# Kernel optimization log

Measured on AMD Instinct MI355X. Metric: run time of the kernel, lower is better.

## Reference

```python
import jax, jax.numpy as jnp
import numpy as np

N = 38332          # poi_len - 1 nodes
POI_LEN = 38333
GF = 64            # graph_features
POI_DIM = 128
C = 128            # gcn_channel
L = 4              # gcn_layers
OUT = 128          # graph_out_dim
E = N * 16         # edges (avg degree 16)
IN_DIM = POI_DIM * GF // 2 + GF // 2  # 4128


def leaky(x, s):
    return jnp.where(x >= 0, x, s * x)


def _gcn(x, W, b, src, dst):
    # PyG GCNConv: lin -> symmetric deg^{-1/2} norm over self-loop graph -> scatter-sum + bias
    h = x @ W
    deg = jax.ops.segment_sum(jnp.ones(src.shape[0], h.dtype), dst, num_segments=N)
    dinv = jnp.where(deg > 0, jax.lax.rsqrt(deg), 0.0)
    norm = dinv[src] * dinv[dst]
    return jax.ops.segment_sum(h[src] * norm[:, None], dst, num_segments=N) + b


def _gat(x, W, a_src, a_dst, b, src, dst):
    # PyG GATConv (heads=1): per-edge LeakyReLU(0.2) logits, softmax over incoming edges
    h = x @ W
    als = h @ a_src            # [N]
    ald = h @ a_dst            # [N]
    e = leaky(als[src] + ald[dst], 0.2)   # [E+N]
    m = jax.ops.segment_max(e, dst, num_segments=N)
    ex = jnp.exp(e - m[dst])
    s = jax.ops.segment_sum(ex, dst, num_segments=N)
    alpha = ex / s[dst]
    return jax.ops.segment_sum(h[src] * alpha[:, None], dst, num_segments=N) + b


def _gnorm(x, w, b, ms, eps=1e-5):
    # PyG GraphNorm over the single graph (node axis)
    mean = x.mean(axis=0)
    out = x - ms * mean
    var = (out * out).mean(axis=0)
    return w * out * jax.lax.rsqrt(var + eps) + b


def setup_inputs() -> dict:
    key = jax.random.key(0)
    ks = jax.random.split(key, 20)
    d = {}
    d["poi"] = jax.random.randint(ks[0], (N, GF // 2), 0, POI_LEN, dtype=jnp.int32)
    d["distance"] = jax.random.uniform(ks[1], (N, GF // 2), dtype=jnp.float32)
    d["edge_index"] = jax.random.randint(ks[2], (2, E), 0, N, dtype=jnp.int32)
    d["emb_table"] = jax.random.normal(ks[3], (POI_LEN, POI_DIM), dtype=jnp.float32) * 0.05
    d["W_in"] = jax.random.normal(ks[4], (IN_DIM, C), dtype=jnp.float32) * 0.02
    d["b_in"] = jnp.zeros((C,), jnp.float32)
    d["gcn_W"] = jax.random.normal(ks[5], (L, C, C), dtype=jnp.float32) * 0.05
    d["gcn_b"] = jnp.zeros((L, C), jnp.float32)
    d["norm_w"] = jnp.ones((L, C), jnp.float32)
    d["norm_b"] = jnp.zeros((L, C), jnp.float32)
    d["norm_ms"] = jnp.ones((L, C), jnp.float32)
    d["gat_W"] = jax.random.normal(ks[6], (L, C, C), dtype=jnp.float32) * 0.05
    d["gat_asrc"] = jax.random.normal(ks[7], (L, C), dtype=jnp.float32) * 0.05
    d["gat_adst"] = jax.random.normal(ks[8], (L, C), dtype=jnp.float32) * 0.05
    d["gat_b"] = jnp.zeros((L, C), jnp.float32)
    d["W_out"] = jax.random.normal(ks[9], (C, 1), dtype=jnp.float32) * 0.05
    d["b_out"] = jnp.zeros((1,), jnp.float32)
    d["fc1_W"] = jax.random.normal(ks[10], (N, 128), dtype=jnp.float32) * 0.01
    d["fc1_b"] = jnp.zeros((128,), jnp.float32)
    d["fc2_W"] = jax.random.normal(ks[11], (128, OUT), dtype=jnp.float32) * 0.05
    d["fc2_b"] = jnp.zeros((OUT,), jnp.float32)
    return d


def reference(poi, distance, edge_index, emb_table, W_in, b_in, gcn_W, gcn_b,
              norm_w, norm_b, norm_ms, gat_W, gat_asrc, gat_adst, gat_b,
              W_out, b_out, fc1_W, fc1_b, fc2_W, fc2_b):
    loops = jnp.arange(N, dtype=edge_index.dtype)
    src = jnp.concatenate([edge_index[0], loops])   # self loops (PyG default)
    dst = jnp.concatenate([edge_index[1], loops])
    # feature assembly: emb(poi) flattened || distance
    x = jnp.concatenate([emb_table[poi].reshape(N, -1), distance], axis=1)  # [N, 4128]
    x = leaky(_gcn(x, W_in, b_in, src, dst), 0.01)
    for i in range(L):  # GcnUnit: GCN->norm->lrelu->res, GAT->norm->lrelu->res (shared norm params)
        t = _gnorm(_gcn(x, gcn_W[i], gcn_b[i], src, dst), norm_w[i], norm_b[i], norm_ms[i])
        x = x + leaky(t, 0.01)
        t = _gnorm(_gat(x, gat_W[i], gat_asrc[i], gat_adst[i], gat_b[i], src, dst),
                   norm_w[i], norm_b[i], norm_ms[i])
        x = x + leaky(t, 0.01)
    x = leaky(_gcn(x, W_out, b_out, src, dst), 0.01).reshape(-1)  # [N]
    h = leaky(x @ fc1_W + fc1_b, 0.01)
    return h @ fc2_W + fc2_b  # [128]
```

## Files before the change

### kernel.cpp

```cpp
#include <hip/hip_runtime.h>


typedef _Float16 f16;
typedef f16 f16x8 __attribute__((ext_vector_type(8)));
typedef f16 f16x4 __attribute__((ext_vector_type(4)));
typedef f16 f16x2 __attribute__((ext_vector_type(2)));
typedef float f32x4 __attribute__((ext_vector_type(4)));

__device__ __forceinline__ float lrelu(float x, float s){ return x>=0.f? x : s*x; }

__global__ __launch_bounds__(256) void k_deg(const int* __restrict__ dst,
                                             int* __restrict__ deg, int E) {
  int i = blockIdx.x * 256 + threadIdx.x;
  if (i < E) atomicAdd(&deg[dst[i]], 1);
}

__global__ __launch_bounds__(1024) void k_scan1(const int* __restrict__ deg,
    int* __restrict__ row_ptr, int* __restrict__ bsum, float* __restrict__ dinv, int n) {
  int b = blockIdx.x, t = threadIdx.x, i = b * 1024 + t;
  __shared__ int sd[1024];
  int v = (i < n) ? deg[i] : 0;
  if (i < n) dinv[i] = rsqrtf((float)(v + 1));
  sd[t] = v;
  __syncthreads();
  for (int off = 1; off < 1024; off <<= 1) {
    int o = (t >= off) ? sd[t - off] : 0;
    __syncthreads();
    sd[t] += o;
    __syncthreads();
  }
  if (i < n) row_ptr[i + 1] = sd[t];
  if (t == 1023) bsum[b] = sd[1023];
  if (b == 0 && t == 0) row_ptr[0] = 0;
}

__global__ __launch_bounds__(64) void k_scan2(int* __restrict__ bsum, int nb) {
  int lane = threadIdx.x;
  int v = (lane < nb) ? bsum[lane] : 0;
  int x = v;
  for (int off = 1; off < 64; off <<= 1) {
    int o = __shfl_up(x, off, 64);
    if (lane >= off) x += o;
  }
  if (lane < nb) bsum[lane] = x - v;
}

__global__ __launch_bounds__(256) void k_scan3(int* __restrict__ row_ptr,
                                               const int* __restrict__ bsum, int n) {
  int i = blockIdx.x * 256 + threadIdx.x;
  if (i < n) row_ptr[i + 1] += bsum[i >> 10];
}

__global__ __launch_bounds__(256) void k_fill(const int* __restrict__ src,
                                              const int* __restrict__ dst,
                                              const int* __restrict__ row_ptr,
                                              const float* __restrict__ dinv,
                                              int* __restrict__ fill,
                                              int* __restrict__ csr,
                                              float* __restrict__ csrw, int E) {
  int i = blockIdx.x * 256 + threadIdx.x;
  if (i < E) {
    int d = dst[i], s = src[i];
    int pos = row_ptr[d] + atomicAdd(&fill[d], 1);
    csr[pos] = s;
    csrw[pos] = dinv[d] * dinv[s];
  }
}

__global__ __launch_bounds__(256) void k_conv_emb(const float* __restrict__ src,
                                                  f16* __restrict__ dst, int total4) {
  int i = blockIdx.x * 256 + threadIdx.x;
  if (i >= total4) return;
  float4 v = ((const float4*)src)[i];
  f16x4 o = { (f16)v.x, (f16)v.y, (f16)v.z, (f16)v.w };
  ((f16x4*)dst)[i] = o;
}

__global__ __launch_bounds__(256) void k_pack_w(const float* __restrict__ W,
    f16* __restrict__ hi, int kb_total) {
  int idx = blockIdx.x * 256 + threadIdx.x;
  int c = idx & 127, kb = idx >> 7;
  if (kb >= kb_total) return;
  f16x8 hv;
#pragma unroll
  for (int j = 0; j < 8; j++) hv[j] = (f16)W[(size_t)(kb*8 + j) * 128 + c];
  ((f16x8*)hi)[idx] = hv;
}

__global__ __launch_bounds__(256) void k_pack_w8(const float* __restrict__ gcnW,
    const float* __restrict__ gatW, f16* __restrict__ hi, f16* __restrict__ lo) {
  int mat = blockIdx.y;
  const float* W = (mat < 4) ? gcnW + (size_t)mat * 16384 : gatW + (size_t)(mat - 4) * 16384;
  int idx = blockIdx.x * 256 + threadIdx.x;
  int c = idx & 127, kb = idx >> 7;
  f16x8 hv, lv;
#pragma unroll
  for (int j = 0; j < 8; j++) {
    float v = W[(size_t)(kb*8 + j) * 128 + c];
    f16 h = (f16)v;
    hv[j] = h; lv[j] = (f16)(v - (float)h);
  }
  ((f16x8*)hi)[mat * 2048 + idx] = hv;
  ((f16x8*)lo)[mat * 2048 + idx] = lv;
}

#define APAD 152
__global__ __launch_bounds__(512) void k_mfma_embed(const int* __restrict__ poi,
    const float* __restrict__ dist, const f16* __restrict__ eh,
    const f16* __restrict__ wh, f16* __restrict__ H16, int n) {
  __shared__ __attribute__((aligned(16))) char smem[49152];
  int* poi_s = (int*)smem;
  f16* aS    = (f16*)(smem + 8192);
  f16* OT    = (f16*)smem;
  float* F   = (float*)(smem + 16384);
  int tid = threadIdx.x;
  int bn = blockIdx.x * 64;
  int half = tid >> 8;
  int t2 = tid & 255;
  int ln = t2 >> 2, qt = t2 & 3;
  int xrow = bn + ln; if (xrow > n - 1) xrow = n - 1;
  {
#pragma unroll
    for (int jj = 0; jj < 4; jj++)
      poi_s[half * 1024 + (qt * 4 + jj) * 64 + ln] =
        poi[(size_t)xrow * 32 + half * 16 + qt * 4 + jj];
  }
  int w2 = (tid >> 6) & 3, lane = tid & 63;
  int q = lane >> 4, l15 = lane & 15;
  int mtb = (w2 & 1) * 2;
  int ntb = (w2 >> 1) * 4;
  f16* aH = aS + half * 64 * APAD;
  f32x4 acc[2][4];
#pragma unroll
  for (int a = 0; a < 2; a++)
#pragma unroll
    for (int b = 0; b < 4; b++) { acc[a][b][0]=0.f; acc[a][b][1]=0.f; acc[a][b][2]=0.f; acc[a][b][3]=0.f; }
  __syncthreads();

  f16x8 r0, r1, r2, r3;
  {
    const f16* srcp = eh + (size_t)poi_s[half * 1024 + ln] * 128 + qt * 32;
    r0 = *(const f16x8*)(srcp);      r1 = *(const f16x8*)(srcp + 8);
    r2 = *(const f16x8*)(srcp + 16); r3 = *(const f16x8*)(srcp + 24);
  }

#pragma unroll 1
  for (int j = 0; j < 16; j++) {
    __syncthreads();
    f16* wp = aH + ln * APAD + qt * 32;
    *(f16x8*)(wp) = r0; *(f16x8*)(wp + 8) = r1;
    *(f16x8*)(wp + 16) = r2; *(f16x8*)(wp + 24) = r3;
    if (j + 1 < 16) {
      const f16* srcp = eh + (size_t)poi_s[half * 1024 + (j + 1) * 64 + ln] * 128 + qt * 32;
      r0 = *(const f16x8*)(srcp);      r1 = *(const f16x8*)(srcp + 8);
      r2 = *(const f16x8*)(srcp + 16); r3 = *(const f16x8*)(srcp + 24);
    }
    __syncthreads();
#pragma unroll
    for (int kcl = 0; kcl < 4; kcl++) {
      f16x8 a_h[2];
#pragma unroll
      for (int mi = 0; mi < 2; mi++)
        a_h[mi] = *(const f16x8*)(aH + ((mtb + mi) * 16 + l15) * APAD + kcl * 32 + q * 8);
      int kb = (half * 16 + j) * 16 + kcl * 4 + q;
#pragma unroll
      for (int ni = 0; ni < 4; ni++) {
        f16x8 bh = *(const f16x8*)(wh + ((size_t)kb * 128 + (ntb + ni) * 16 + l15) * 8);
#pragma unroll
        for (int mi = 0; mi < 2; mi++)
          acc[mi][ni] = __builtin_amdgcn_mfma_f32_16x16x32_f16(a_h[mi], bh, acc[mi][ni], 0, 0, 0);
      }
    }
  }
  if (half) {
    int nc0 = bn + (mtb + 0) * 16 + l15; if (nc0 > n - 1) nc0 = n - 1;
    int nc1 = bn + (mtb + 1) * 16 + l15; if (nc1 > n - 1) nc1 = n - 1;
    f16x8 ad[2];
#pragma unroll
    for (int mi = 0; mi < 2; mi++) {
      int nc = mi ? nc1 : nc0;
      const float* dp = dist + (size_t)nc * 32 + q * 8;
      float4 d0 = *(const float4*)dp, d1 = *(const float4*)(dp + 4);
      ad[mi][0]=(f16)d0.x; ad[mi][1]=(f16)d0.y; ad[mi][2]=(f16)d0.z; ad[mi][3]=(f16)d0.w;
      ad[mi][4]=(f16)d1.x; ad[mi][5]=(f16)d1.y; ad[mi][6]=(f16)d1.z; ad[mi][7]=(f16)d1.w;
    }
    int kb = 512 + q;
#pragma unroll
    for (int ni = 0; ni < 4; ni++) {
      f16x8 bh = *(const f16x8*)(wh + ((size_t)kb * 128 + (ntb + ni) * 16 + l15) * 8);
#pragma unroll
      for (int mi = 0; mi < 2; mi++)
        acc[mi][ni] = __builtin_amdgcn_mfma_f32_16x16x32_f16(ad[mi], bh, acc[mi][ni], 0, 0, 0);
    }
  }
  __syncthreads();
  if (half) {
#pragma unroll
    for (int mi = 0; mi < 2; mi++)
#pragma unroll
      for (int ni = 0; ni < 4; ni++)
#pragma unroll
        for (int r = 0; r < 4; r++)
          F[((mtb + mi) * 16 + q * 4 + r) * 128 + (ntb + ni) * 16 + l15] = acc[mi][ni][r];
  }
  __syncthreads();
  if (!half) {
#pragma unroll
    for (int mi = 0; mi < 2; mi++)
#pragma unroll
      for (int ni = 0; ni < 4; ni++)
#pragma unroll
        for (int r = 0; r < 4; r++) {
          int o = ((mtb + mi) * 16 + q * 4 + r) * 128 + (ntb + ni) * 16 + l15;
          OT[o] = (f16)(acc[mi][ni][r] + F[o]);
        }
  }
  __syncthreads();
#pragma unroll
  for (int ch = 0; ch < 2; ch++) {
    int c1024 = tid + ch * 512;
    int row = c1024 >> 4, c8 = c1024 & 15;
    if (bn + row < n)
      *(f16x8*)(H16 + (size_t)(bn + row) * 128 + c8 * 8) = *(const f16x8*)(OT + row * 128 + c8 * 8);
  }
}

#define LPAD 136
__global__ __launch_bounds__(256) void k_mfma_lin(const f16* __restrict__ XH,
    const f16* __restrict__ wh, const f16* __restrict__ wl,
    f16* __restrict__ H16, int n,
    const float* __restrict__ asrc, const float* __restrict__ adst,
    float* __restrict__ als, float* __restrict__ ald,
    const float* __restrict__ yres, const float* __restrict__ ps,
    const float* __restrict__ pq, const float* __restrict__ nw,
    const float* __restrict__ nbb, const float* __restrict__ nms,
    float* __restrict__ xf) {
  __shared__ __attribute__((aligned(16))) char smem[64 * LPAD * 2 + 3072];
  f16* aS = (f16*)smem;
  f16* ot = (f16*)smem;
  float* dsrc = (float*)(smem + 16384);
  float* ddst = (float*)(smem + 16896);
  float* scf  = (float*)(smem + 17408);
  float* shf  = scf + 128;
  float* sst1 = (float*)(smem + 18432);
  float* sst2 = sst1 + 256;
  int tid = threadIdx.x;
  int bn = blockIdx.x * 64;
  int ln = tid >> 2, qt = tid & 3;
  int w = tid >> 6, lane = tid & 63;
  int q = lane >> 4, l15 = lane & 15;
  int mtb = (w & 1) * 2;
  int ntb = (w >> 1) * 4;
  f16* wp = aS + ln * LPAD + qt * 32;
  if (yres) {
    {
      int c = tid & 127, hf = tid >> 7;
      float S = 0.f, Q = 0.f;
      for (int s = hf; s < 128; s += 2) { S += ps[s * 128 + c]; Q += pq[s * 128 + c]; }
      sst1[tid] = S; sst2[tid] = Q;
      __syncthreads();
      if (hf == 0) {
        double Sd = (double)sst1[c] + (double)sst1[c + 128];
        double Qd = (double)sst2[c] + (double)sst2[c + 128];
        double invn = 1.0 / (double)n;
        double mean = Sd * invn;
        double mt = (double)nms[c] * mean;
        double var = Qd * invn - 2.0 * mt * mean + mt * mt;
        float rstd = rsqrtf((float)var + 1e-5f);
        float sc = nw[c] * rstd;
        scf[c] = sc;
        shf[c] = nbb[c] - sc * (float)mt;
      }
      __syncthreads();
    }
    int row = bn + ln;
    if (row < n) {
      const float4* yp = (const float4*)(yres + (size_t)row * 128 + qt * 32);
      float4* xp = (float4*)(xf + (size_t)row * 128 + qt * 32);
      const float4* scp = (const float4*)(scf + qt * 32);
      const float4* shp = (const float4*)(shf + qt * 32);
#pragma unroll
      for (int jj = 0; jj < 8; jj++) {
        float4 yv = yp[jj], xv = xp[jj], sc = scp[jj], sh = shp[jj];
        xv.x += lrelu(sc.x * yv.x + sh.x, 0.01f);
        xv.y += lrelu(sc.y * yv.y + sh.y, 0.01f);
        xv.z += lrelu(sc.z * yv.z + sh.z, 0.01f);
        xv.w += lrelu(sc.w * yv.w + sh.w, 0.01f);
        xp[jj] = xv;
        f16x4 o = { (f16)xv.x, (f16)xv.y, (f16)xv.z, (f16)xv.w };
        *(f16x4*)(wp + jj * 4) = o;
      }
    } else {
      f16x8 z = {};
#pragma unroll
      for (int jj = 0; jj < 4; jj++) *(f16x8*)(wp + jj * 8) = z;
    }
  } else {
    int xrow = bn + ln; if (xrow > n - 1) xrow = n - 1;
    const f16* srcp = XH + (size_t)xrow * 128 + qt * 32;
    *(f16x8*)(wp)      = *(const f16x8*)(srcp);
    *(f16x8*)(wp + 8)  = *(const f16x8*)(srcp + 8);
    *(f16x8*)(wp + 16) = *(const f16x8*)(srcp + 16);
    *(f16x8*)(wp + 24) = *(const f16x8*)(srcp + 24);
  }
  float av[4], bv[4];
  if (asrc) {
#pragma unroll
    for (int ni = 0; ni < 4; ni++) {
      av[ni] = asrc[(ntb + ni) * 16 + l15];
      bv[ni] = adst[(ntb + ni) * 16 + l15];
    }
  }
  f32x4 acc[2][4];
#pragma unroll
  for (int a = 0; a < 2; a++)
#pragma unroll
    for (int b = 0; b < 4; b++) { acc[a][b][0]=0.f; acc[a][b][1]=0.f; acc[a][b][2]=0.f; acc[a][b][3]=0.f; }
  __syncthreads();
#pragma unroll
  for (int kcl = 0; kcl < 4; kcl++) {
    f16x8 a_h[2];
#pragma unroll
    for (int mi = 0; mi < 2; mi++)
      a_h[mi] = *(const f16x8*)(aS + ((mtb + mi) * 16 + l15) * LPAD + kcl * 32 + q * 8);
    int kb = kcl * 4 + q;
#pragma unroll
    for (int ni = 0; ni < 4; ni++) {
      size_t boff = ((size_t)kb * 128 + (ntb + ni) * 16 + l15) * 8;
      f16x8 bh = *(const f16x8*)(wh + boff);
      f16x8 bl = *(const f16x8*)(wl + boff);
#pragma unroll
      for (int mi = 0; mi < 2; mi++) {
        acc[mi][ni] = __builtin_amdgcn_mfma_f32_16x16x32_f16(a_h[mi], bh, acc[mi][ni], 0, 0, 0);
        acc[mi][ni] = __builtin_amdgcn_mfma_f32_16x16x32_f16(a_h[mi], bl, acc[mi][ni], 0, 0, 0);
      }
    }
  }
  __syncthreads();
  if (asrc) {
#pragma unroll
    for (int mi = 0; mi < 2; mi++)
#pragma unroll
      for (int r = 0; r < 4; r++) {
        float ps2 = 0.f, pd = 0.f;
#pragma unroll
        for (int ni = 0; ni < 4; ni++) { ps2 += acc[mi][ni][r] * av[ni]; pd += acc[mi][ni][r] * bv[ni]; }
#pragma unroll
        for (int msk = 8; msk > 0; msk >>= 1) {
          ps2 += __shfl_xor(ps2, msk, 64);
          pd += __shfl_xor(pd, msk, 64);
        }
        if (l15 == 0) {
          int row = (mtb + mi) * 16 + q * 4 + r;
          dsrc[row * 2 + (w >> 1)] = ps2;
          ddst[row * 2 + (w >> 1)] = pd;
        }
      }
  }
#pragma unroll
  for (int mi = 0; mi < 2; mi++)
#pragma unroll
    for (int ni = 0; ni < 4; ni++)
#pragma unroll
      for (int r = 0; r < 4; r++)
        ot[((mtb + mi) * 16 + q * 4 + r) * 128 + (ntb + ni) * 16 + l15] = (f16)acc[mi][ni][r];
  __syncthreads();
  if (bn + ln < n) {
    f16* dst = H16 + (size_t)(bn + ln) * 128 + qt * 32;
    const f16* srcp = ot + ln * 128 + qt * 32;
#pragma unroll
    for (int jj = 0; jj < 4; jj++)
      *(f16x8*)(dst + jj * 8) = *(const f16x8*)(srcp + jj * 8);
  }
  if (asrc && tid < 64 && bn + tid < n) {
    als[bn + tid] = dsrc[tid * 2] + dsrc[tid * 2 + 1];
    ald[bn + tid] = ddst[tid * 2] + ddst[tid * 2 + 1];
  }
}

__global__ __launch_bounds__(256) void k_gcn_agg16(const f16x2* __restrict__ H2,
    const float* __restrict__ dinv, const int* __restrict__ row_ptr,
    const int* __restrict__ csr, const float* __restrict__ csrw,
    const float* __restrict__ bias,
    float2* __restrict__ out2, f16x2* __restrict__ xh_out, int n, int leaky_flag,
    float* __restrict__ psum, float* __restrict__ psumsq) {
  int w = threadIdx.x >> 6;
  int node = blockIdx.x * 4 + w;
  int lane = threadIdx.x & 63;
  __shared__ float s1[4][128], s2[4][128];
  float vx = 0.f, vy = 0.f;
  if (node < n) {
    int rs = row_ptr[node], re = row_ptr[node + 1];
    int d = re - rs;
    float dn = dinv[node];
    int  sidx = (lane < d) ? csr[rs + lane]  : 0;
    float swt = (lane < d) ? csrw[rs + lane] : 0.f;
    f16x2 sv = H2[(size_t)node * 64 + lane];
    float ax = dn * dn * (float)sv[0], ay = dn * dn * (float)sv[1];
    int dl = d < 64 ? d : 64;
    int dl8 = (dl + 7) & ~7;
    for (int j = 0; j < dl8; j += 8) {
      int ii[8]; float ww[8];
#pragma unroll
      for (int u = 0; u < 8; u++) {
        ii[u] = __shfl(sidx, j + u, 64);
        ww[u] = __shfl(swt,  j + u, 64);
      }
      f16x2 vv[8];
#pragma unroll
      for (int u = 0; u < 8; u++) vv[u] = H2[(size_t)ii[u] * 64 + lane];
#pragma unroll
      for (int u = 0; u < 8; u++) {
        ax += ww[u] * (float)vv[u][0];
        ay += ww[u] * (float)vv[u][1];
      }
    }
    for (int e = rs + 64; e < re; e++) {
      int s = csr[e]; float wv = csrw[e];
      f16x2 v = H2[(size_t)s * 64 + lane];
      ax += wv * (float)v[0]; ay += wv * (float)v[1];
    }
    float2 bvv = ((const float2*)bias)[lane];
    vx = ax + bvv.x; vy = ay + bvv.y;
    if (leaky_flag) { vx = lrelu(vx, 0.01f); vy = lrelu(vy, 0.01f); }
    out2[(size_t)node * 64 + lane] = make_float2(vx, vy);
    if (xh_out) { f16x2 o = { (f16)vx, (f16)vy }; xh_out[(size_t)node * 64 + lane] = o; }
  }
  if (psum) {
    s1[w][2*lane] = vx;  s1[w][2*lane+1] = vy;
    s2[w][2*lane] = vx*vx; s2[w][2*lane+1] = vy*vy;
    __syncthreads();
    int t = threadIdx.x;
    if (t < 128) {
      float S = s1[0][t] + s1[1][t] + s1[2][t] + s1[3][t];
      float Q = s2[0][t] + s2[1][t] + s2[2][t] + s2[3][t];
      int slot = blockIdx.x & 127;
      atomicAdd(&psum[slot * 128 + t], S);
      atomicAdd(&psumsq[slot * 128 + t], Q);
    }
  }
}

__global__ __launch_bounds__(256) void k_gat_agg16(const f16x2* __restrict__ H2,
    const float* __restrict__ als, const float* __restrict__ ald,
    const int* __restrict__ row_ptr, const int* __restrict__ csr,
    const float* __restrict__ bias, float2* __restrict__ y2, int n,
    float* __restrict__ psum, float* __restrict__ psumsq) {
  int w = threadIdx.x >> 6;
  int node = blockIdx.x * 4 + w;
  int lane = threadIdx.x & 63;
  __shared__ float s1[4][128], s2[4][128];
  float vx = 0.f, vy = 0.f;
  if (node < n) {
    int rs = row_ptr[node], re = row_ptr[node + 1];
    int d = re - rs;
    float aldn = ald[node];
    float e_self = lrelu(als[node] + aldn, 0.2f);
    f16x2 sv = H2[(size_t)node * 64 + lane];
    float ax, ay, sm;
    if (d <= 64) {
      int sidx = (lane < d) ? csr[rs + lane] : 0;
      float e_k = (lane < d) ? lrelu(als[sidx] + aldn, 0.2f) : -3.4e38f;
      float tmx = e_k;
      for (int off = 1; off < 64; off <<= 1) tmx = fmaxf(tmx, __shfl_xor(tmx, off, 64));
      float mx = fmaxf(e_self, tmx);
      float g_k = (lane < d) ? __expf(e_k - mx) : 0.f;
      float tsm = g_k;
      for (int off = 1; off < 64; off <<= 1) tsm += __shfl_xor(tsm, off, 64);
      float ws = __expf(e_self - mx);
      sm = tsm + ws;
      ax = ws * (float)sv[0]; ay = ws * (float)sv[1];
      int d8 = (d + 7) & ~7;
      for (int j = 0; j < d8; j += 8) {
        int ii[8]; float gg[8];
#pragma unroll
        for (int u = 0; u < 8; u++) {
          ii[u] = __shfl(sidx, j + u, 64);
          gg[u] = __shfl(g_k,  j + u, 64);
        }
        f16x2 vv[8];
#pragma unroll
        for (int u = 0; u < 8; u++) vv[u] = H2[(size_t)ii[u] * 64 + lane];
#pragma unroll
        for (int u = 0; u < 8; u++) {
          ax += gg[u] * (float)vv[u][0];
          ay += gg[u] * (float)vv[u][1];
        }
      }
    } else {
      float mx = e_self;
      for (int i = rs + lane; i < re; i += 64) mx = fmaxf(mx, lrelu(als[csr[i]] + aldn, 0.2f));
      for (int off = 1; off < 64; off <<= 1) mx = fmaxf(mx, __shfl_xor(mx, off, 64));
      float ws = __expf(e_self - mx);
      sm = ws;
      ax = ws * (float)sv[0]; ay = ws * (float)sv[1];
      for (int i = rs; i < re; i++) {
        int s = csr[i];
        float g = __expf(lrelu(als[s] + aldn, 0.2f) - mx);
        f16x2 v = H2[(size_t)s * 64 + lane];
        sm += g; ax += g*(float)v[0]; ay += g*(float)v[1];
      }
    }
    float inv_s = 1.f / sm;
    float2 bvv = ((const float2*)bias)[lane];
    vx = ax * inv_s + bvv.x; vy = ay * inv_s + bvv.y;
    y2[(size_t)node * 64 + lane] = make_float2(vx, vy);
  }
  s1[w][2*lane] = vx;  s1[w][2*lane+1] = vy;
  s2[w][2*lane] = vx*vx; s2[w][2*lane+1] = vy*vy;
  __syncthreads();
  int t = threadIdx.x;
  if (t < 128) {
    float S = s1[0][t] + s1[1][t] + s1[2][t] + s1[3][t];
    float Q = s2[0][t] + s2[1][t] + s2[2][t] + s2[3][t];
    int slot = blockIdx.x & 127;
    atomicAdd(&psum[slot * 128 + t], S);
    atomicAdd(&psumsq[slot * 128 + t], Q);
  }
}

__global__ __launch_bounds__(256) void k_stats(const float* __restrict__ psum,
    const float* __restrict__ psumsq, const float* __restrict__ w,
    const float* __restrict__ bb, const float* __restrict__ ms,
    float* __restrict__ scaleA, float* __restrict__ shiftA, int n) {
  int t = threadIdx.x, c = t & 127, half = t >> 7;
  float S = 0.f, Q = 0.f;
  for (int s = half; s < 128; s += 2) { S += psum[s * 128 + c]; Q += psumsq[s * 128 + c]; }
  __shared__ float sh[256], sq[256];
  sh[t] = S; sq[t] = Q;
  __syncthreads();
  if (half == 0) {
    double Sd = (double)sh[c] + (double)sh[c + 128];
    double Qd = (double)sq[c] + (double)sq[c + 128];
    double invn = 1.0 / (double)n;
    double mean = Sd * invn;
    double mt = (double)ms[c] * mean;
    double var = Qd * invn - 2.0 * mt * mean + mt * mt;
    float rstd = rsqrtf((float)var + 1e-5f);
    float sc = w[c] * rstd;
    scaleA[c] = sc;
    shiftA[c] = bb[c] - sc * (float)mt;
  }
}

__global__ __launch_bounds__(256) void k_dot1_res(const float* __restrict__ y,
    const float* __restrict__ scA, const float* __restrict__ shA,
    const float* __restrict__ x, const float* __restrict__ wv,
    float* __restrict__ o, int n) {
  int node = blockIdx.x * 4 + (threadIdx.x >> 6);
  int lane = threadIdx.x & 63;
  if (node >= n) return;
  float2 yv = ((const float2*)y)[(size_t)node * 64 + lane];
  float2 xv = ((const float2*)x)[(size_t)node * 64 + lane];
  float2 sc = ((const float2*)scA)[lane];
  float2 sh = ((const float2*)shA)[lane];
  float hx = xv.x + lrelu(sc.x * yv.x + sh.x, 0.01f);
  float hy = xv.y + lrelu(sc.y * yv.y + sh.y, 0.01f);
  float2 v1 = ((const float2*)wv)[lane];
  float s1 = hx * v1.x + hy * v1.y;
  for (int off = 32; off > 0; off >>= 1) s1 += __shfl_down(s1, off, 64);
  if (lane == 0) o[node] = s1;
}

__global__ __launch_bounds__(256) void k_scalar_agg(const float* __restrict__ xsv,
    const float* __restrict__ dinv, const int* __restrict__ row_ptr,
    const int* __restrict__ csr, const float* __restrict__ csrw,
    const float* __restrict__ b_out, float* __restrict__ xout, int n) {
  int i = blockIdx.x * 256 + threadIdx.x;
  if (i >= n) return;
  float dn = dinv[i];
  float acc = dn * dn * xsv[i];
  int re = row_ptr[i + 1];
  for (int e = row_ptr[i]; e < re; e++)
    acc += csrw[e] * xsv[csr[e]];
  xout[i] = lrelu(acc + b_out[0], 0.01f);
}

__global__ __launch_bounds__(256) void k_fc1(const float* __restrict__ xout,
    const float* __restrict__ fw, float* __restrict__ pfc, int n, int chunk) {
  int b = blockIdx.x, t = threadIdx.x;
  int c = t & 127, half = t >> 7;
  int s0 = b * chunk;
  int s1 = s0 + chunk; if (s1 > n) s1 = n;
  float s = 0.f;
  for (int i = s0 + half; i < s1; i += 2) s += xout[i] * fw[(size_t)i * 128 + c];
  __shared__ float sh[256];
  sh[t] = s; __syncthreads();
  if (half == 0) pfc[b * 128 + c] = sh[c] + sh[c + 128];
}

__global__ __launch_bounds__(128) void k_final(const float* __restrict__ pfc,
    const float* __restrict__ b1, const float* __restrict__ fw2,
    const float* __restrict__ b2, float* __restrict__ out) {
  int c = threadIdx.x;
  float s = 0.f;
  for (int b = 0; b < 128; b++) s += pfc[b * 128 + c];
  float hv = lrelu(s + b1[c], 0.01f);
  __shared__ float h1[128];
  h1[c] = hv; __syncthreads();
  float o = b2[c];
  for (int j = 0; j < 128; j++) o += h1[j] * fw2[j * 128 + c];
  out[c] = o;
}

extern "C" void kernel_launch(void* const* d_in, const int* in_sizes, int n_in,
                              void* d_out, int out_size, void* d_ws, size_t ws_size,
                              hipStream_t stream) {
  const int* poi      = (const int*)d_in[0];
  const float* dist   = (const float*)d_in[1];
  const int* ei       = (const int*)d_in[2];
  const float* emb    = (const float*)d_in[3];
  const float* W_in   = (const float*)d_in[4];
  const float* b_in   = (const float*)d_in[5];
  const float* gcn_W  = (const float*)d_in[6];
  const float* gcn_b  = (const float*)d_in[7];
  const float* norm_w = (const float*)d_in[8];
  const float* norm_b = (const float*)d_in[9];
  const float* norm_ms= (const float*)d_in[10];
  const float* gat_W  = (const float*)d_in[11];
  const float* gat_as = (const float*)d_in[12];
  const float* gat_ad = (const float*)d_in[13];
  const float* gat_b  = (const float*)d_in[14];
  const float* W_out  = (const float*)d_in[15];
  const float* b_out  = (const float*)d_in[16];
  const float* fc1_W  = (const float*)d_in[17];
  const float* fc1_b  = (const float*)d_in[18];
  const float* fc2_W  = (const float*)d_in[19];
  const float* fc2_b  = (const float*)d_in[20];

  const int N   = in_sizes[0] / 32;
  const int E   = in_sizes[2] / 2;
  const int POI = in_sizes[3] / 128;
  const int* srcp = ei;
  const int* dstp = ei + E;
  float* out = (float*)d_out;

  char* p = (char*)d_ws;
  auto alloc = [&](size_t bytes) { char* r = p; p += (bytes + 255) & ~(size_t)255; return r; };
  float* x   = (float*)alloc((size_t)N * 128 * 4);
  f16* h16   = (f16*)alloc((size_t)N * 128 * 2);
  f16* xh    = (f16*)alloc((size_t)N * 128 * 2);
  size_t Rneed = (size_t)POI * 128 * 2;
  size_t Ry    = (size_t)N * 128 * 4;
  char* R = alloc(Rneed > Ry ? Rneed : Ry);
  f16* ehalf = (f16*)R;
  float* y   = (float*)R;
  const int KBIN = 4128 / 8;
  f16* wih = (f16*)alloc((size_t)KBIN * 128 * 8 * 2);
  f16* wsh = (f16*)alloc((size_t)8 * 16384 * 2);
  f16* wsl = (f16*)alloc((size_t)8 * 16384 * 2);
  float* dinv   = (float*)alloc((size_t)N * 4);
  float* als    = (float*)alloc((size_t)N * 4);
  float* ald    = (float*)alloc((size_t)N * 4);
  float* xsv    = (float*)alloc((size_t)N * 4);
  float* xout   = (float*)alloc((size_t)N * 4);
  float* statsbuf = (float*)alloc((size_t)32 * 16384 * 4);
  float* pfc    = (float*)alloc(128 * 128 * 4);
  float* scaleA = (float*)alloc(128 * 4);
  float* shiftA = (float*)alloc(128 * 4);
  int* deg     = (int*)alloc((size_t)N * 2 * 4);
  int* fill    = deg + N;
  int* row_ptr = (int*)alloc(((size_t)N + 1) * 4);
  int* csr     = (int*)alloc((size_t)E * 4);
  float* csrw  = (float*)alloc((size_t)E * 4);
  int* bsum    = (int*)alloc(64 * 4);

  const int chunk = (N + 127) / 128;
  const int gblocks = (N + 63) / 64;
  const int eblocks = (E + 255) / 256;
  const int nwb = (N + 3) / 4;
  const int nb1024 = (N + 1023) / 1024;

  hipMemsetAsync(deg, 0, sizeof(int) * 2 * (size_t)N, stream);
  hipMemsetAsync(statsbuf, 0, (size_t)32 * 16384 * 4, stream);
  k_deg<<<eblocks, 256, 0, stream>>>(dstp, deg, E);
  k_scan1<<<nb1024, 1024, 0, stream>>>(deg, row_ptr, bsum, dinv, N);
  k_scan2<<<1, 64, 0, stream>>>(bsum, nb1024);
  k_scan3<<<(N + 255) / 256, 256, 0, stream>>>(row_ptr, bsum, N);
  k_fill<<<eblocks, 256, 0, stream>>>(srcp, dstp, row_ptr, dinv, fill, csr, csrw, E);

  int et4 = POI * 128 / 4;
  k_conv_emb<<<(et4 + 255) / 256, 256, 0, stream>>>(emb, ehalf, et4);
  k_pack_w<<<(KBIN * 128 + 255) / 256, 256, 0, stream>>>(W_in, wih, KBIN);
  k_pack_w8<<<dim3(8, 8), 256, 0, stream>>>(gcn_W, gat_W, wsh, wsl);

  k_mfma_embed<<<gblocks, 512, 0, stream>>>(poi, dist, ehalf, wih, h16, N);
  k_gcn_agg16<<<nwb, 256, 0, stream>>>((const f16x2*)h16, dinv, row_ptr, csr, csrw, b_in,
                                       (float2*)x, (f16x2*)xh, N, 1, nullptr, nullptr);

  for (int l = 0; l < 4; l++) {
    const f16* gh = wsh + (size_t)l * 16384;
    const f16* gl = wsl + (size_t)l * 16384;
    const f16* th = wsh + (size_t)(4 + l) * 16384;
    const f16* tl = wsl + (size_t)(4 + l) * 16384;
    float* ps0 = statsbuf + (size_t)(4 * l) * 16384;
    float* pq0 = ps0 + 16384;
    float* ps1 = ps0 + 2 * 16384;
    float* pq1 = ps0 + 3 * 16384;
    if (l == 0)
      k_mfma_lin<<<gblocks, 256, 0, stream>>>(xh, gh, gl, h16, N,
          nullptr, nullptr, nullptr, nullptr,
          nullptr, nullptr, nullptr, nullptr, nullptr, nullptr, nullptr);
    else {
      float* ps1p = statsbuf + (size_t)(4 * (l - 1) + 2) * 16384;
      float* pq1p = ps1p + 16384;
      k_mfma_lin<<<gblocks, 256, 0, stream>>>(nullptr, gh, gl, h16, N,
          nullptr, nullptr, nullptr, nullptr,
          y, ps1p, pq1p, norm_w + (l - 1) * 128, norm_b + (l - 1) * 128,
          norm_ms + (l - 1) * 128, x);
    }
    k_gcn_agg16<<<nwb, 256, 0, stream>>>((const f16x2*)h16, dinv, row_ptr, csr, csrw,
                                         gcn_b + l * 128, (float2*)y, (f16x2*)nullptr, N, 0,
                                         ps0, pq0);
    k_mfma_lin<<<gblocks, 256, 0, stream>>>(nullptr, th, tl, h16, N,
        gat_as + l * 128, gat_ad + l * 128, als, ald,
        y, ps0, pq0, norm_w + l * 128, norm_b + l * 128, norm_ms + l * 128, x);
    k_gat_agg16<<<nwb, 256, 0, stream>>>((const f16x2*)h16, als, ald, row_ptr, csr,
                                         gat_b + l * 128, (float2*)y, N, ps1, pq1);
  }

  {
    float* ps1 = statsbuf + (size_t)(4 * 3 + 2) * 16384;
    float* pq1 = ps1 + 16384;
    k_stats<<<1, 256, 0, stream>>>(ps1, pq1, norm_w + 3 * 128, norm_b + 3 * 128,
                                   norm_ms + 3 * 128, scaleA, shiftA, N);
  }
  k_dot1_res<<<nwb, 256, 0, stream>>>(y, scaleA, shiftA, x, W_out, xsv, N);
  k_scalar_agg<<<(N + 255) / 256, 256, 0, stream>>>(xsv, dinv, row_ptr, csr, csrw, b_out, xout, N);
  k_fc1<<<128, 256, 0, stream>>>(xout, fc1_W, pfc, N, chunk);
  k_final<<<1, 128, 0, stream>>>(pfc, fc1_b, fc2_W, fc2_b, out);
}
```

Before: 981.2 us.

## Split H16 into two column-half planes and aggregate each half in separate blocks

```diff
diff --git a/kernel.cpp b/kernel.cpp
--- a/kernel.cpp
+++ b/kernel.cpp
@@ -220,8 +220,10 @@
   for (int ch = 0; ch < 2; ch++) {
     int c1024 = tid + ch * 512;
     int row = c1024 >> 4, c8 = c1024 & 15;
-    if (bn + row < n)
-      *(f16x8*)(H16 + (size_t)(bn + row) * 128 + c8 * 8) = *(const f16x8*)(OT + row * 128 + c8 * 8);
+    if (bn + row < n) {
+      f16* dstp = H16 + (size_t)(c8 >> 3) * ((size_t)n * 64) + (size_t)(bn + row) * 64 + (c8 & 7) * 8;
+      *(f16x8*)dstp = *(const f16x8*)(OT + row * 128 + c8 * 8);
+    }
   }
 }
 
@@ -366,11 +368,11 @@
         ot[((mtb + mi) * 16 + q * 4 + r) * 128 + (ntb + ni) * 16 + l15] = (f16)acc[mi][ni][r];
   __syncthreads();
   if (bn + ln < n) {
-    f16* dst = H16 + (size_t)(bn + ln) * 128 + qt * 32;
     const f16* srcp = ot + ln * 128 + qt * 32;
+    f16* dstp = H16 + (size_t)(qt >> 1) * ((size_t)n * 64) + (size_t)(bn + ln) * 64 + (qt & 1) * 32;
 #pragma unroll
     for (int jj = 0; jj < 4; jj++)
-      *(f16x8*)(dst + jj * 8) = *(const f16x8*)(srcp + jj * 8);
+      *(f16x8*)(dstp + jj * 8) = *(const f16x8*)(srcp + jj * 8);
   }
   if (asrc && tid < 64 && bn + tid < n) {
     als[bn + tid] = dsrc[tid * 2] + dsrc[tid * 2 + 1];
@@ -378,16 +380,20 @@
   }
 }
 
-__global__ __launch_bounds__(256) void k_gcn_agg16(const f16x2* __restrict__ H2,
+__global__ __launch_bounds__(256) void k_gcn_agg16(const f16* __restrict__ H,
     const float* __restrict__ dinv, const int* __restrict__ row_ptr,
     const int* __restrict__ csr, const float* __restrict__ csrw,
     const float* __restrict__ bias,
-    float2* __restrict__ out2, f16x2* __restrict__ xh_out, int n, int leaky_flag,
-    float* __restrict__ psum, float* __restrict__ psumsq) {
+    float* __restrict__ yout, f16* __restrict__ xh_out, int n, int nwb,
+    int leaky_flag, float* __restrict__ psum, float* __restrict__ psumsq) {
   int w = threadIdx.x >> 6;
-  int node = blockIdx.x * 4 + w;
+  int bx = blockIdx.x;
+  int pass = (bx >= nwb) ? 1 : 0;
+  int node = (bx - pass * nwb) * 4 + w;
   int lane = threadIdx.x & 63;
-  __shared__ float s1[4][128], s2[4][128];
+  int l5 = lane >> 5, m = lane & 31;
+  const f16x2* Hh2 = (const f16x2*)(H + (size_t)pass * ((size_t)n * 64));
+  __shared__ float s1[4][64], s2[4][64];
   float vx = 0.f, vy = 0.f;
   if (node < n) {
     int rs = row_ptr[node], re = row_ptr[node + 1];
@@ -395,68 +401,86 @@
     float dn = dinv[node];
     int  sidx = (lane < d) ? csr[rs + lane]  : 0;
     float swt = (lane < d) ? csrw[rs + lane] : 0.f;
-    f16x2 sv = H2[(size_t)node * 64 + lane];
-    float ax = dn * dn * (float)sv[0], ay = dn * dn * (float)sv[1];
+    f16x2 sv = Hh2[(size_t)node * 32 + m];
+    float selfw = l5 ? 0.f : dn * dn;
+    float ax = selfw * (float)sv[0], ay = selfw * (float)sv[1];
     int dl = d < 64 ? d : 64;
-    int dl8 = (dl + 7) & ~7;
-    for (int j = 0; j < dl8; j += 8) {
+    int rounds = (dl + 1) >> 1;
+    int r8v = (rounds + 7) & ~7;
+    for (int r = 0; r < r8v; r += 8) {
       int ii[8]; float ww[8];
 #pragma unroll
       for (int u = 0; u < 8; u++) {
-        ii[u] = __shfl(sidx, j + u, 64);
-        ww[u] = __shfl(swt,  j + u, 64);
+        int src = 2 * (r + u) + l5;
+        ii[u] = __shfl(sidx, src, 64);
+        ww[u] = __shfl(swt,  src, 64);
       }
       f16x2 vv[8];
 #pragma unroll
-      for (int u = 0; u < 8; u++) vv[u] = H2[(size_t)ii[u] * 64 + lane];
+      for (int u = 0; u < 8; u++) vv[u] = Hh2[(size_t)ii[u] * 32 + m];
 #pragma unroll
       for (int u = 0; u < 8; u++) {
         ax += ww[u] * (float)vv[u][0];
         ay += ww[u] * (float)vv[u][1];
       }
     }
-    for (int e = rs + 64; e < re; e++) {
-      int s = csr[e]; float wv = csrw[e];
-      f16x2 v = H2[(size_t)s * 64 + lane];
+    for (int e = rs + 64; e < re; e += 2) {
+      int ee = e + l5;
+      int s = (ee < re) ? csr[ee] : 0;
+      float wv = (ee < re) ? csrw[ee] : 0.f;
+      f16x2 v = Hh2[(size_t)s * 32 + m];
       ax += wv * (float)v[0]; ay += wv * (float)v[1];
     }
-    float2 bvv = ((const float2*)bias)[lane];
+    ax += __shfl_xor(ax, 32, 64);
+    ay += __shfl_xor(ay, 32, 64);
+    float2 bvv = ((const float2*)(bias + pass * 64))[m];
     vx = ax + bvv.x; vy = ay + bvv.y;
     if (leaky_flag) { vx = lrelu(vx, 0.01f); vy = lrelu(vy, 0.01f); }
-    out2[(size_t)node * 64 + lane] = make_float2(vx, vy);
-    if (xh_out) { f16x2 o = { (f16)vx, (f16)vy }; xh_out[(size_t)node * 64 + lane] = o; }
+    if (l5 == 0) {
+      ((float2*)(yout + (size_t)node * 128 + pass * 64))[m] = make_float2(vx, vy);
+      if (xh_out) {
+        f16x2 o = { (f16)vx, (f16)vy };
+        ((f16x2*)xh_out)[(size_t)node * 64 + pass * 32 + m] = o;
+      }
+    }
   }
   if (psum) {
-    s1[w][2*lane] = vx;  s1[w][2*lane+1] = vy;
-    s2[w][2*lane] = vx*vx; s2[w][2*lane+1] = vy*vy;
+    if (l5 == 0) {
+      s1[w][2*m] = vx;  s1[w][2*m+1] = vy;
+      s2[w][2*m] = vx*vx; s2[w][2*m+1] = vy*vy;
+    }
     __syncthreads();
     int t = threadIdx.x;
-    if (t < 128) {
+    if (t < 64) {
       float S = s1[0][t] + s1[1][t] + s1[2][t] + s1[3][t];
       float Q = s2[0][t] + s2[1][t] + s2[2][t] + s2[3][t];
-      int slot = blockIdx.x & 127;
-      atomicAdd(&psum[slot * 128 + t], S);
-      atomicAdd(&psumsq[slot * 128 + t], Q);
-    }
-  }
-}
-
-__global__ __launch_bounds__(256) void k_gat_agg16(const f16x2* __restrict__ H2,
+      int slot = bx & 127;
+      atomicAdd(&psum[slot * 128 + pass * 64 + t], S);
+      atomicAdd(&psumsq[slot * 128 + pass * 64 + t], Q);
+    }
+  }
+}
+
+__global__ __launch_bounds__(256) void k_gat_agg16(const f16* __restrict__ H,
     const float* __restrict__ als, const float* __restrict__ ald,
     const int* __restrict__ row_ptr, const int* __restrict__ csr,
-    const float* __restrict__ bias, float2* __restrict__ y2, int n,
+    const float* __restrict__ bias, float* __restrict__ yout, int n, int nwb,
     float* __restrict__ psum, float* __restrict__ psumsq) {
   int w = threadIdx.x >> 6;
-  int node = blockIdx.x * 4 + w;
+  int bx = blockIdx.x;
+  int pass = (bx >= nwb) ? 1 : 0;
+  int node = (bx - pass * nwb) * 4 + w;
   int lane = threadIdx.x & 63;
-  __shared__ float s1[4][128], s2[4][128];
+  int l5 = lane >> 5, m = lane & 31;
+  const f16x2* Hh2 = (const f16x2*)(H + (size_t)pass * ((size_t)n * 64));
+  __shared__ float s1[4][64], s2[4][64];
   float vx = 0.f, vy = 0.f;
   if (node < n) {
     int rs = row_ptr[node], re = row_ptr[node + 1];
     int d = re - rs;
     float aldn = ald[node];
     float e_self = lrelu(als[node] + aldn, 0.2f);
-    f16x2 sv = H2[(size_t)node * 64 + lane];
+    f16x2 sv = Hh2[(size_t)node * 32 + m];
     float ax, ay, sm;
     if (d <= 64) {
       int sidx = (lane < d) ? csr[rs + lane] : 0;
@@ -469,18 +493,21 @@
       for (int off = 1; off < 64; off <<= 1) tsm += __shfl_xor(tsm, off, 64);
       float ws = __expf(e_self - mx);
       sm = tsm + ws;
-      ax = ws * (float)sv[0]; ay = ws * (float)sv[1];
-      int d8 = (d + 7) & ~7;
-      for (int j = 0; j < d8; j += 8) {
+      float selfw = l5 ? 0.f : ws;
+      ax = selfw * (float)sv[0]; ay = selfw * (float)sv[1];
+      int rounds = (d + 1) >> 1;
+      int r8v = (rounds + 7) & ~7;
+      for (int r = 0; r < r8v; r += 8) {
         int ii[8]; float gg[8];
 #pragma unroll
         for (int u = 0; u < 8; u++) {
-          ii[u] = __shfl(sidx, j + u, 64);
-          gg[u] = __shfl(g_k,  j + u, 64);
+          int src = 2 * (r + u) + l5;
+          ii[u] = __shfl(sidx, src, 64);
+          gg[u] = __shfl(g_k,  src, 64);
         }
         f16x2 vv[8];
 #pragma unroll
-        for (int u = 0; u < 8; u++) vv[u] = H2[(size_t)ii[u] * 64 + lane];
+        for (int u = 0; u < 8; u++) vv[u] = Hh2[(size_t)ii[u] * 32 + m];
 #pragma unroll
         for (int u = 0; u < 8; u++) {
           ax += gg[u] * (float)vv[u][0];
@@ -492,30 +519,39 @@
       for (int i = rs + lane; i < re; i += 64) mx = fmaxf(mx, lrelu(als[csr[i]] + aldn, 0.2f));
       for (int off = 1; off < 64; off <<= 1) mx = fmaxf(mx, __shfl_xor(mx, off, 64));
       float ws = __expf(e_self - mx);
-      sm = ws;
-      ax = ws * (float)sv[0]; ay = ws * (float)sv[1];
-      for (int i = rs; i < re; i++) {
-        int s = csr[i];
-        float g = __expf(lrelu(als[s] + aldn, 0.2f) - mx);
-        f16x2 v = H2[(size_t)s * 64 + lane];
-        sm += g; ax += g*(float)v[0]; ay += g*(float)v[1];
-      }
-    }
+      float selfw = l5 ? 0.f : ws;
+      ax = selfw * (float)sv[0]; ay = selfw * (float)sv[1];
+      float smA = 0.f;
+      for (int e = rs; e < re; e += 2) {
+        int ee = e + l5;
+        int s = (ee < re) ? csr[ee] : 0;
+        float g = (ee < re) ? __expf(lrelu(als[s] + aldn, 0.2f) - mx) : 0.f;
+        f16x2 v = Hh2[(size_t)s * 32 + m];
+        smA += g; ax += g * (float)v[0]; ay += g * (float)v[1];
+      }
+      smA += __shfl_xor(smA, 32, 64);
+      sm = ws + smA;
+    }
+    ax += __shfl_xor(ax, 32, 64);
+    ay += __shfl_xor(ay, 32, 64);
     float inv_s = 1.f / sm;
-    float2 bvv = ((const float2*)bias)[lane];
+    float2 bvv = ((const float2*)(bias + pass * 64))[m];
     vx = ax * inv_s + bvv.x; vy = ay * inv_s + bvv.y;
-    y2[(size_t)node * 64 + lane] = make_float2(vx, vy);
-  }
-  s1[w][2*lane] = vx;  s1[w][2*lane+1] = vy;
-  s2[w][2*lane] = vx*vx; s2[w][2*lane+1] = vy*vy;
+    if (l5 == 0)
+      ((float2*)(yout + (size_t)node * 128 + pass * 64))[m] = make_float2(vx, vy);
+  }
+  if (l5 == 0) {
+    s1[w][2*m] = vx;  s1[w][2*m+1] = vy;
+    s2[w][2*m] = vx*vx; s2[w][2*m+1] = vy*vy;
+  }
   __syncthreads();
   int t = threadIdx.x;
-  if (t < 128) {
+  if (t < 64) {
     float S = s1[0][t] + s1[1][t] + s1[2][t] + s1[3][t];
     float Q = s2[0][t] + s2[1][t] + s2[2][t] + s2[3][t];
-    int slot = blockIdx.x & 127;
-    atomicAdd(&psum[slot * 128 + t], S);
-    atomicAdd(&psumsq[slot * 128 + t], Q);
+    int slot = bx & 127;
+    atomicAdd(&psum[slot * 128 + pass * 64 + t], S);
+    atomicAdd(&psumsq[slot * 128 + pass * 64 + t], Q);
   }
 }
 
@@ -685,8 +721,8 @@
   k_pack_w8<<<dim3(8, 8), 256, 0, stream>>>(gcn_W, gat_W, wsh, wsl);
 
   k_mfma_embed<<<gblocks, 512, 0, stream>>>(poi, dist, ehalf, wih, h16, N);
-  k_gcn_agg16<<<nwb, 256, 0, stream>>>((const f16x2*)h16, dinv, row_ptr, csr, csrw, b_in,
-                                       (float2*)x, (f16x2*)xh, N, 1, nullptr, nullptr);
+  k_gcn_agg16<<<2 * nwb, 256, 0, stream>>>(h16, dinv, row_ptr, csr, csrw, b_in,
+                                           x, xh, N, nwb, 1, nullptr, nullptr);
 
   for (int l = 0; l < 4; l++) {
     const f16* gh = wsh + (size_t)l * 16384;
@@ -709,14 +745,14 @@
           y, ps1p, pq1p, norm_w + (l - 1) * 128, norm_b + (l - 1) * 128,
           norm_ms + (l - 1) * 128, x);
     }
-    k_gcn_agg16<<<nwb, 256, 0, stream>>>((const f16x2*)h16, dinv, row_ptr, csr, csrw,
-                                         gcn_b + l * 128, (float2*)y, (f16x2*)nullptr, N, 0,
-                                         ps0, pq0);
+    k_gcn_agg16<<<2 * nwb, 256, 0, stream>>>(h16, dinv, row_ptr, csr, csrw,
+                                             gcn_b + l * 128, y, (f16*)nullptr, N, nwb, 0,
+                                             ps0, pq0);
     k_mfma_lin<<<gblocks, 256, 0, stream>>>(nullptr, th, tl, h16, N,
         gat_as + l * 128, gat_ad + l * 128, als, ald,
         y, ps0, pq0, norm_w + l * 128, norm_b + l * 128, norm_ms + l * 128, x);
-    k_gat_agg16<<<nwb, 256, 0, stream>>>((const f16x2*)h16, als, ald, row_ptr, csr,
-                                         gat_b + l * 128, (float2*)y, N, ps1, pq1);
+    k_gat_agg16<<<2 * nwb, 256, 0, stream>>>(h16, als, ald, row_ptr, csr,
+                                             gat_b + l * 128, y, N, nwb, ps1, pq1);
   }
 
   {
```

Result: slower. 1.057 ms (+7.7%).
